# Kernel optimization log

Measured on AMD Instinct MI355X. Metric: run time of the kernel, lower is better.

Reference implementation:

```python
import jax, jax.numpy as jnp
import numpy as np

EPS = 1e-5

def _layernorm(x, gamma, beta):
    mu = jnp.mean(x, axis=-1, keepdims=True)
    var = jnp.var(x, axis=-1, keepdims=True)
    return (x - mu) * jax.lax.rsqrt(var + EPS) * gamma + beta

def setup_inputs() -> dict:
    key = jax.random.key(0)
    ks = jax.random.split(key, 8)
    B, I, H = 8192, 1024, 1024
    s_w = 1.0 / np.sqrt(I)
    s_u = 1.0 / np.sqrt(H)
    return {
        "x": jax.random.normal(ks[0], (B, I), jnp.float32),
        "h": jax.random.normal(ks[1], (B, H), jnp.float32),
        "c": jax.random.normal(ks[2], (B, H), jnp.float32),
        "W_w": jax.random.uniform(ks[3], (I, 4 * H), jnp.float32, -s_w, s_w),
        "W_b": jax.random.uniform(ks[4], (4 * H,), jnp.float32, -s_w, s_w),
        "U_w": jax.random.uniform(ks[5], (H, 4 * H), jnp.float32, -s_u, s_u),
        "ln_g_gamma": jnp.ones((4 * H,), jnp.float32),
        "ln_g_beta": jnp.zeros((4 * H,), jnp.float32),
        "ln_c_gamma": jnp.ones((H,), jnp.float32),
        "ln_c_beta": jnp.zeros((H,), jnp.float32),
    }

def reference(x, h, c, W_w, W_b, U_w, ln_g_gamma, ln_g_beta, ln_c_gamma, ln_c_beta):
    gates_x = x @ W_w + W_b            # [B, 4H]
    gates_h = h @ U_w                  # [B, 4H]
    gates = gates_x + gates_h + gates_x * gates_h  # multiplicative integration
    gates = _layernorm(gates, ln_g_gamma, ln_g_beta)
    i, f, g, o = jnp.split(gates, 4, axis=-1)
    i = jax.nn.sigmoid(i)
    f = jax.nn.sigmoid(f)
    o = jax.nn.sigmoid(o)
    g = jnp.tanh(g)
    c_new = f * c + i * g
    c_new = _layernorm(c_new, ln_c_gamma, ln_c_beta)
    h_new = o * jnp.tanh(c_new)
    return (h_new, h_new, c_new)
```

## Files before the change

### kernel.cpp

```cpp
#include <hip/hip_runtime.h>
#include <hip/hip_fp16.h>
#include <cstdint>


#define MB (1024ull * 1024ull)

typedef short bf16x8 __attribute__((ext_vector_type(8)));
typedef float f32x4  __attribute__((ext_vector_type(4)));

__device__ __forceinline__ bool bf16_mode(const void* g1) {
    return ((const unsigned short*)g1)[0] == 0x3F80u;
}
__device__ __forceinline__ float b2f(unsigned short u) {
    union { unsigned int i; float f; } v; v.i = ((unsigned int)u) << 16; return v.f;
}
__device__ __forceinline__ unsigned short f2b(float f) {
    unsigned int i = __float_as_uint(f);
    unsigned int r = (i + 0x7FFFu + ((i >> 16) & 1u)) >> 16;
    return (unsigned short)r;
}
__device__ __forceinline__ unsigned short f2h(float f) {
    __half h = __float2half_rn(f);
    return *(unsigned short*)&h;
}
__device__ __forceinline__ void uph8(uint4 v, float* o) {
    unsigned int w[4] = { v.x, v.y, v.z, v.w };
#pragma unroll
    for (int q = 0; q < 4; ++q) {
        __half2 h = *(__half2*)&w[q];
        float2 f = __half22float2(h);
        o[2 * q] = f.x; o[2 * q + 1] = f.y;
    }
}
__device__ __forceinline__ void up4(uint2 v, float* o) {
    o[0] = __uint_as_float(v.x << 16);
    o[1] = __uint_as_float(v.x & 0xFFFF0000u);
    o[2] = __uint_as_float(v.y << 16);
    o[3] = __uint_as_float(v.y & 0xFFFF0000u);
}
__device__ __forceinline__ unsigned int pack2(unsigned short a, unsigned short b) {
    return (unsigned int)a | ((unsigned int)b << 16);
}
__device__ __forceinline__ void ld4(const void* p, size_t idx, bool isbf, float* o) {
    if (isbf) up4(*(const uint2*)((const unsigned short*)p + idx), o);
    else { float4 v = *(const float4*)((const float*)p + idx); o[0]=v.x; o[1]=v.y; o[2]=v.z; o[3]=v.w; }
}
__device__ __forceinline__ float fast_sigmoid(float z) { return 1.f / (1.f + __expf(-z)); }
__device__ __forceinline__ float fast_tanh(float z)    { return 1.f - 2.f / (__expf(2.f * z) + 1.f); }

__device__ __forceinline__ void load_lds16(const unsigned short* g, unsigned short* l) {
    __builtin_amdgcn_global_load_lds(
        (const __attribute__((address_space(1))) unsigned int*)g,
        (__attribute__((address_space(3))) unsigned int*)l,
        16, 0, 0);
}

__global__ __launch_bounds__(256)
void prep_weights(const void* __restrict__ Ww, const void* __restrict__ Uw,
                  const void* __restrict__ g1,
                  unsigned short* __restrict__ Wt, unsigned short* __restrict__ Ut)
{
    const bool isbf = bf16_mode(g1);
    const void* src = blockIdx.z ? Uw : Ww;
    unsigned short* dst = blockIdx.z ? Ut : Wt;
    __shared__ unsigned short tile[64][68];
    const int t  = threadIdx.x;
    const int tx = t & 15;
    const int ty = t >> 4;
    const int bx = blockIdx.x * 64;
    const int by = blockIdx.y * 64;
    if (isbf) {
        const unsigned short* s = (const unsigned short*)src;
#pragma unroll
        for (int it = 0; it < 4; ++it) {
            const int r = ty + it * 16;
            uint2 v = *(const uint2*)(s + (size_t)(by + r) * 4096 + bx + tx * 4);
            tile[r][tx * 4 + 0] = (unsigned short)(v.x & 0xFFFFu);
            tile[r][tx * 4 + 1] = (unsigned short)(v.x >> 16);
            tile[r][tx * 4 + 2] = (unsigned short)(v.y & 0xFFFFu);
            tile[r][tx * 4 + 3] = (unsigned short)(v.y >> 16);
        }
    } else {
        const float* s = (const float*)src;
#pragma unroll
        for (int it = 0; it < 4; ++it) {
            const int r = ty + it * 16;
            float4 v = *(const float4*)(s + (size_t)(by + r) * 4096 + bx + tx * 4);
            tile[r][tx * 4 + 0] = f2b(v.x);
            tile[r][tx * 4 + 1] = f2b(v.y);
            tile[r][tx * 4 + 2] = f2b(v.z);
            tile[r][tx * 4 + 3] = f2b(v.w);
        }
    }
    __syncthreads();
#pragma unroll
    for (int it = 0; it < 4; ++it) {
        const int rn = ty + it * 16;
        const int ck = tx * 4;
        uint2 w;
        w.x = pack2(tile[ck + 0][rn], tile[ck + 1][rn]);
        w.y = pack2(tile[ck + 2][rn], tile[ck + 3][rn]);
        *(uint2*)(dst + (size_t)(bx + rn) * 1024 + by + ck) = w;
    }
}

__global__ __launch_bounds__(256)
void prep_xh(const void* __restrict__ X, const void* __restrict__ Hs,
             const void* __restrict__ g1, void* __restrict__ outb)
{
    if (bf16_mode(g1)) return;
    const float* src = (blockIdx.y == 0) ? (const float*)X : (const float*)Hs;
    unsigned short* dst = (unsigned short*)((char*)outb + (blockIdx.y == 0 ? 48 * MB : 80 * MB));
    const size_t i0 = ((size_t)blockIdx.x * 256 + threadIdx.x) * 8;
    float4 a = *(const float4*)(src + i0);
    float4 b = *(const float4*)(src + i0 + 4);
    uint4 o;
    o.x = pack2(f2b(a.x), f2b(a.y));
    o.y = pack2(f2b(a.z), f2b(a.w));
    o.z = pack2(f2b(b.x), f2b(b.y));
    o.w = pack2(f2b(b.z), f2b(b.w));
    *(uint4*)(dst + i0) = o;
}

__global__ __launch_bounds__(512, 2)
void milstm_gemm(const void* __restrict__ Xraw, const void* __restrict__ Hraw,
                 const void* __restrict__ g1, const void* __restrict__ outb,
                 const unsigned short* __restrict__ Wt,
                 const unsigned short* __restrict__ Ut,
                 unsigned short* __restrict__ Gx, unsigned short* __restrict__ Gh,
                 int m0)
{
    const bool isbf = bf16_mode(g1);
    const int  z    = blockIdx.z;
    const unsigned short* A = z
        ? (isbf ? (const unsigned short*)Hraw : (const unsigned short*)((const char*)outb + 80 * MB))
        : (isbf ? (const unsigned short*)Xraw : (const unsigned short*)((const char*)outb + 48 * MB));
    const unsigned short* Bm = z ? Ut : Wt;
    unsigned short* Gout = z ? Gh : Gx;

    __shared__ __align__(16) unsigned short lds[4][2][8192];

    const int t    = threadIdx.x;
    const int wave = t >> 6;
    const int lane = t & 63;
    const int quad = lane >> 4;
    const int l16  = lane & 15;
    const int wm2  = wave >> 2;
    const int wn4  = wave & 3;

    const int nwg  = gridDim.x * gridDim.y;
    const int wgid = blockIdx.y * gridDim.x + blockIdx.x;
    const int swz  = (wgid & 7) * (nwg >> 3) + (wgid >> 3);
    const int bm   = (swz >> 4) * 256;
    const int bn   = (swz & 15) * 256;

    const int kbsw = (((t & 3) ^ ((t >> 3) & 3)) * 8);
    const unsigned short* sa0 = A  + (size_t)(m0 + bm + (t >> 2)) * 1024 + kbsw;
    const unsigned short* sb0 = Bm + (size_t)(bn + (t >> 2)) * 1024 + kbsw;

#define STAGE(tile, buf) do {                                        \
        const int ko_ = (tile) * 32;                                 \
        load_lds16(sa0 + ko_,          &lds[buf][0][t * 8]);         \
        load_lds16(sa0 + 131072 + ko_, &lds[buf][0][4096 + t * 8]);  \
        load_lds16(sb0 + ko_,          &lds[buf][1][t * 8]);         \
        load_lds16(sb0 + 131072 + ko_, &lds[buf][1][4096 + t * 8]);  \
    } while (0)

    const int kread = (quad ^ ((l16 >> 1) & 3)) * 8;
    const int raoff = (wm2 * 128 + l16) * 32 + kread;
    const int rboff = (wn4 * 64 + l16) * 32 + kread;

    f32x4 acc[8][4] = {};

    STAGE(0, 0);
    STAGE(1, 1);
    STAGE(2, 2);

    for (int q = 0; q < 32; ++q) {
        const int buf = q & 3;
        asm volatile("s_waitcnt vmcnt(8)" ::: "memory");
        __builtin_amdgcn_s_barrier();
        __builtin_amdgcn_sched_barrier(0);
        STAGE((q + 3) & 31, (q + 3) & 3);

        const unsigned short* pA = &lds[buf][0][0];
        const unsigned short* pB = &lds[buf][1][0];
        bf16x8 b[4], a[8];
#pragma unroll
        for (int ni = 0; ni < 4; ++ni) b[ni] = *(const bf16x8*)(pB + rboff + ni * 512);
#pragma unroll
        for (int mi = 0; mi < 8; ++mi) a[mi] = *(const bf16x8*)(pA + raoff + mi * 512);

        __builtin_amdgcn_s_setprio(1);
#pragma unroll
        for (int mi = 0; mi < 8; ++mi)
#pragma unroll
            for (int ni = 0; ni < 4; ++ni)
                acc[mi][ni] = __builtin_amdgcn_mfma_f32_16x16x32_bf16(a[mi], b[ni], acc[mi][ni], 0, 0, 0);
        __builtin_amdgcn_s_setprio(0);
    }
#undef STAGE

    const int col0 = bn + wn4 * 64 + l16;
#pragma unroll
    for (int mi = 0; mi < 8; ++mi) {
        const int row0 = bm + wm2 * 128 + mi * 16 + quad * 4;
#pragma unroll
        for (int ni = 0; ni < 4; ++ni) {
            const int col = col0 + ni * 16;
#pragma unroll
            for (int r = 0; r < 4; ++r)
                Gout[(size_t)(row0 + r) * 4096 + col] = f2h(acc[mi][ni][r]);
        }
    }
}

__global__ __launch_bounds__(256)
void milstm_cell(const unsigned short* __restrict__ Gx,
                 const unsigned short* __restrict__ Gh,
                 const void* __restrict__ Wbr,
                 const void* __restrict__ C,
                 const void* __restrict__ g1, const void* __restrict__ b1,
                 const void* __restrict__ g2, const void* __restrict__ b2,
                 void* __restrict__ outb, int m0)
{
    const bool isbf = bf16_mode(g1);
    const int lrow = blockIdx.x;
    const int row  = m0 + lrow;
    const int tid  = threadIdx.x;
    const int lane = tid & 63;
    const int wave = tid >> 6;
    const uint4* gx4 = (const uint4*)(Gx + (size_t)lrow * 4096);
    const uint4* gh4 = (const uint4*)(Gh + (size_t)lrow * 4096);

    __shared__ __align__(16) float srow[4096];
    __shared__ float red[16];

    float s = 0.f, ss = 0.f;
#pragma unroll
    for (int u = 0; u < 2; ++u) {
        const int gbase = (tid * 2 + u) * 8;
        float fx[8], fh[8], bb[8];
        uph8(gx4[tid * 2 + u], fx);
        uph8(gh4[tid * 2 + u], fh);
        ld4(Wbr, gbase, isbf, bb);
        ld4(Wbr, gbase + 4, isbf, bb + 4);
        float g[8];
#pragma unroll
        for (int k = 0; k < 8; ++k) {
            const float ax = fx[k] + bb[k];
            const float v  = ax + fh[k] + ax * fh[k];
            g[k] = v;
            s  += v;
            ss += v * v;
        }
        *(float4*)&srow[gbase]     = make_float4(g[0], g[1], g[2], g[3]);
        *(float4*)&srow[gbase + 4] = make_float4(g[4], g[5], g[6], g[7]);
    }
#pragma unroll
    for (int off = 32; off > 0; off >>= 1) {
        s  += __shfl_xor(s, off, 64);
        ss += __shfl_xor(ss, off, 64);
    }
    if (lane == 0) { red[wave] = s; red[8 + wave] = ss; }
    __syncthreads();
    s  = red[0] + red[1] + red[2] + red[3];
    ss = red[8] + red[9] + red[10] + red[11];
    const float mu   = s * (1.f / 4096.f);
    const float rstd = rsqrtf(fmaxf(ss * (1.f / 4096.f) - mu * mu, 0.f) + 1e-5f);

    const int j0 = tid * 4;
    float xi[4], xf[4], xg[4], cc[4];
    float G1[4], B1[4], ii[4], cn[4], ov[4];

    { float4 v = *(const float4*)&srow[j0];        xi[0]=v.x; xi[1]=v.y; xi[2]=v.z; xi[3]=v.w; }
    { float4 v = *(const float4*)&srow[1024 + j0]; xf[0]=v.x; xf[1]=v.y; xf[2]=v.z; xf[3]=v.w; }
    { float4 v = *(const float4*)&srow[2048 + j0]; xg[0]=v.x; xg[1]=v.y; xg[2]=v.z; xg[3]=v.w; }
    { float4 v = *(const float4*)&srow[3072 + j0]; ov[0]=v.x; ov[1]=v.y; ov[2]=v.z; ov[3]=v.w; }
    ld4(C, (size_t)row * 1024 + j0, isbf, cc);

    ld4(g1, j0, isbf, G1); ld4(b1, j0, isbf, B1);
#pragma unroll
    for (int q = 0; q < 4; ++q) ii[q] = fast_sigmoid((xi[q] - mu) * rstd * G1[q] + B1[q]);
    ld4(g1, 1024 + j0, isbf, G1); ld4(b1, 1024 + j0, isbf, B1);
#pragma unroll
    for (int q = 0; q < 4; ++q) xf[q] = fast_sigmoid((xf[q] - mu) * rstd * G1[q] + B1[q]);
    ld4(g1, 2048 + j0, isbf, G1); ld4(b1, 2048 + j0, isbf, B1);
#pragma unroll
    for (int q = 0; q < 4; ++q) xg[q] = fast_tanh((xg[q] - mu) * rstd * G1[q] + B1[q]);
    ld4(g1, 3072 + j0, isbf, G1); ld4(b1, 3072 + j0, isbf, B1);
#pragma unroll
    for (int q = 0; q < 4; ++q) ov[q] = fast_sigmoid((ov[q] - mu) * rstd * G1[q] + B1[q]);
#pragma unroll
    for (int q = 0; q < 4; ++q) cn[q] = xf[q] * cc[q] + ii[q] * xg[q];

    float s2  = cn[0] + cn[1] + cn[2] + cn[3];
    float ss2 = cn[0]*cn[0] + cn[1]*cn[1] + cn[2]*cn[2] + cn[3]*cn[3];
#pragma unroll
    for (int off = 32; off > 0; off >>= 1) {
        s2  += __shfl_xor(s2, off, 64);
        ss2 += __shfl_xor(ss2, off, 64);
    }
    if (lane == 0) { red[4 + wave] = s2; red[12 + wave] = ss2; }
    __syncthreads();
    s2  = red[4]  + red[5]  + red[6]  + red[7];
    ss2 = red[12] + red[13] + red[14] + red[15];
    const float mu2   = s2 * (1.f / 1024.f);
    const float rstd2 = rsqrtf(fmaxf(ss2 * (1.f / 1024.f) - mu2 * mu2, 0.f) + 1e-5f);

    ld4(g2, j0, isbf, G1);
    ld4(b2, j0, isbf, B1);

    float hv[4], cv[4];
#pragma unroll
    for (int q = 0; q < 4; ++q) {
        cv[q] = (cn[q] - mu2) * rstd2 * G1[q] + B1[q];
        hv[q] = ov[q] * fast_tanh(cv[q]);
    }

    const size_t BH = (size_t)8192 * 1024;
    if (isbf) {
        unsigned short* out = (unsigned short*)outb;
        uint2 hb, cb;
        hb.x = pack2(f2b(hv[0]), f2b(hv[1])); hb.y = pack2(f2b(hv[2]), f2b(hv[3]));
        cb.x = pack2(f2b(cv[0]), f2b(cv[1])); cb.y = pack2(f2b(cv[2]), f2b(cv[3]));
        *(uint2*)(out + (size_t)row * 1024 + j0)          = hb;
        *(uint2*)(out + BH + (size_t)row * 1024 + j0)     = hb;
        *(uint2*)(out + 2 * BH + (size_t)row * 1024 + j0) = cb;
    } else {
        float* out = (float*)outb;
        float4 hf = { hv[0], hv[1], hv[2], hv[3] };
        float4 cf = { cv[0], cv[1], cv[2], cv[3] };
        *(float4*)(out + (size_t)row * 1024 + j0)          = hf;
        *(float4*)(out + BH + (size_t)row * 1024 + j0)     = hf;
        *(float4*)(out + 2 * BH + (size_t)row * 1024 + j0) = cf;
    }
}

extern "C" void kernel_launch(void* const* d_in, const int* in_sizes, int n_in,
                              void* d_out, int out_size, void* d_ws, size_t ws_size,
                              hipStream_t stream)
{
    const void* X  = d_in[0];
    const void* Hh = d_in[1];
    const void* C  = d_in[2];
    const void* Ww = d_in[3];
    const void* Wb = d_in[4];
    const void* Uw = d_in[5];
    const void* g1 = d_in[6];
    const void* b1 = d_in[7];
    const void* g2 = d_in[8];
    const void* b2 = d_in[9];

    const int P  = (ws_size >= 144 * MB) ? 1 : ((ws_size >= 80 * MB) ? 2 : 4);
    const int MR = 8192 / P;
    const size_t gsz = (size_t)MR * 4096;
    unsigned short* Gx = (unsigned short*)d_ws;
    unsigned short* Gh = Gx + gsz;
    unsigned short* Wt = Gh + gsz;
    unsigned short* Ut = Wt + (size_t)4096 * 1024;

    prep_weights<<<dim3(64, 16, 2), 256, 0, stream>>>(Ww, Uw, g1, Wt, Ut);
    prep_xh<<<dim3(4096, 2), 256, 0, stream>>>(X, Hh, g1, d_out);

    for (int ph = 0; ph < P; ++ph) {
        const int m0 = ph * MR;
        milstm_gemm<<<dim3(16, MR / 256, 2), 512, 0, stream>>>(
            X, Hh, g1, d_out, Wt, Ut, Gx, Gh, m0);
        milstm_cell<<<dim3(MR), 256, 0, stream>>>(
            Gx, Gh, Wb, C, g1, b1, g2, b2, d_out, m0);
    }
}
```

Measured before the change: 408.6 us.

## Restructure GEMM main loop into 8-phase ping-pong schedule with 64-wide K tiles

```diff
diff --git a/kernel.cpp b/kernel.cpp
--- a/kernel.cpp
+++ b/kernel.cpp
@@ -138,15 +138,16 @@
     const unsigned short* Bm = z ? Ut : Wt;
     unsigned short* Gout = z ? Gh : Gx;
 
-    __shared__ __align__(16) unsigned short lds[4][2][8192];
+    __shared__ __align__(16) unsigned short ldsA[2][2][8192];
+    __shared__ __align__(16) unsigned short ldsB[2][2][8192];
 
     const int t    = threadIdx.x;
     const int wave = t >> 6;
     const int lane = t & 63;
     const int quad = lane >> 4;
     const int l16  = lane & 15;
-    const int wm2  = wave >> 2;
-    const int wn4  = wave & 3;
+    const int wm   = wave >> 2;
+    const int wn   = wave & 3;
 
     const int nwg  = gridDim.x * gridDim.y;
     const int wgid = blockIdx.y * gridDim.x + blockIdx.x;
@@ -154,57 +155,119 @@
     const int bm   = (swz >> 4) * 256;
     const int bn   = (swz & 15) * 256;
 
-    const int kbsw = (((t & 3) ^ ((t >> 3) & 3)) * 8);
-    const unsigned short* sa0 = A  + (size_t)(m0 + bm + (t >> 2)) * 1024 + kbsw;
-    const unsigned short* sb0 = Bm + (size_t)(bn + (t >> 2)) * 1024 + kbsw;
-
-#define STAGE(tile, buf) do {                                        \
-        const int ko_ = (tile) * 32;                                 \
-        load_lds16(sa0 + ko_,          &lds[buf][0][t * 8]);         \
-        load_lds16(sa0 + 131072 + ko_, &lds[buf][0][4096 + t * 8]);  \
-        load_lds16(sb0 + ko_,          &lds[buf][1][t * 8]);         \
-        load_lds16(sb0 + 131072 + ko_, &lds[buf][1][4096 + t * 8]);  \
+    const int gls = (((t & 7) ^ ((t >> 3) & 7)) * 8);
+    const unsigned short* pA = A  + (size_t)(m0 + bm + (t >> 3)) * 1024 + gls;
+    const unsigned short* pB = Bm + (size_t)(bn + (t >> 3)) * 1024 + gls;
+
+#define ST_A(DB, H, KO) do {                                                  \
+        load_lds16(pA + (H) * 131072 + (KO),         &ldsA[DB][H][t * 8]);    \
+        load_lds16(pA + (H) * 131072 + 65536 + (KO), &ldsA[DB][H][4096 + t * 8]); \
     } while (0)
-
-    const int kread = (quad ^ ((l16 >> 1) & 3)) * 8;
-    const int raoff = (wm2 * 128 + l16) * 32 + kread;
-    const int rboff = (wn4 * 64 + l16) * 32 + kread;
+#define ST_B(DB, H, KO) do {                                                  \
+        load_lds16(pB + (H) * 131072 + (KO),         &ldsB[DB][H][t * 8]);    \
+        load_lds16(pB + (H) * 131072 + 65536 + (KO), &ldsB[DB][H][4096 + t * 8]); \
+    } while (0)
+
+    const int gp0 = ((quad)     ^ (l16 & 7)) * 8;
+    const int gp1 = ((4 + quad) ^ (l16 & 7)) * 8;
+    const unsigned short* bA0 = &ldsA[0][wm][0] + l16 * 64;
+    const unsigned short* bA1 = &ldsA[1][wm][0] + l16 * 64;
+    const unsigned short* bB0 = &ldsB[0][wn >> 1][0] + (wn & 1) * 4096 + l16 * 64;
+    const unsigned short* bB1 = &ldsB[1][wn >> 1][0] + (wn & 1) * 4096 + l16 * 64;
+
+#define LD_AF(BASE) do { _Pragma("unroll")                                    \
+        for (int j = 0; j < 4; ++j) {                                         \
+            aF[j * 2 + 0] = *(const bf16x8*)((BASE) + j * 1024 + gp0);        \
+            aF[j * 2 + 1] = *(const bf16x8*)((BASE) + j * 1024 + gp1);        \
+        } } while (0)
+#define LD_BF(BASE, DST) do { _Pragma("unroll")                               \
+        for (int n = 0; n < 2; ++n) {                                         \
+            DST[n * 2 + 0] = *(const bf16x8*)((BASE) + n * 1024 + gp0);       \
+            DST[n * 2 + 1] = *(const bf16x8*)((BASE) + n * 1024 + gp1);       \
+        } } while (0)
+
+#define BAR()   __builtin_amdgcn_s_barrier()
+#define LGKM0() do { asm volatile("s_waitcnt lgkmcnt(0)" ::: "memory");       \
+                     __builtin_amdgcn_sched_barrier(0); } while (0)
+#define MFMA16(MBASE, NBASE, BV) do {                                         \
+        __builtin_amdgcn_s_setprio(1);                                        \
+        _Pragma("unroll")                                                     \
+        for (int j = 0; j < 4; ++j)                                           \
+            _Pragma("unroll")                                                 \
+            for (int n = 0; n < 2; ++n)                                       \
+                _Pragma("unroll")                                             \
+                for (int ks = 0; ks < 2; ++ks)                                \
+                    acc[(MBASE) + j][(NBASE) + n] =                           \
+                        __builtin_amdgcn_mfma_f32_16x16x32_bf16(              \
+                            aF[j * 2 + ks], BV[n * 2 + ks],                   \
+                            acc[(MBASE) + j][(NBASE) + n], 0, 0, 0);          \
+        __builtin_amdgcn_s_setprio(0);                                        \
+    } while (0)
 
     f32x4 acc[8][4] = {};
-
-    STAGE(0, 0);
-    STAGE(1, 1);
-    STAGE(2, 2);
-
-    for (int q = 0; q < 32; ++q) {
-        const int buf = q & 3;
-        asm volatile("s_waitcnt vmcnt(8)" ::: "memory");
-        __builtin_amdgcn_s_barrier();
-        __builtin_amdgcn_sched_barrier(0);
-        STAGE((q + 3) & 31, (q + 3) & 3);
-
-        const unsigned short* pA = &lds[buf][0][0];
-        const unsigned short* pB = &lds[buf][1][0];
-        bf16x8 b[4], a[8];
-#pragma unroll
-        for (int ni = 0; ni < 4; ++ni) b[ni] = *(const bf16x8*)(pB + rboff + ni * 512);
-#pragma unroll
-        for (int mi = 0; mi < 8; ++mi) a[mi] = *(const bf16x8*)(pA + raoff + mi * 512);
-
-        __builtin_amdgcn_s_setprio(1);
-#pragma unroll
-        for (int mi = 0; mi < 8; ++mi)
-#pragma unroll
-            for (int ni = 0; ni < 4; ++ni)
-                acc[mi][ni] = __builtin_amdgcn_mfma_f32_16x16x32_bf16(a[mi], b[ni], acc[mi][ni], 0, 0, 0);
-        __builtin_amdgcn_s_setprio(0);
-    }
-#undef STAGE
-
-    const int col0 = bn + wn4 * 64 + l16;
+    bf16x8 aF[8], bL[4], bH[4];
+
+    ST_A(0, 0, 0);  ST_B(0, 0, 0);  ST_B(0, 1, 0);  ST_A(0, 1, 0);
+    ST_A(1, 0, 64); ST_B(1, 0, 64); ST_B(1, 1, 64);
+    asm volatile("s_waitcnt vmcnt(6)" ::: "memory");
+    BAR();
+
+    for (int i = 0; i < 8; ++i) {
+        const int kt1 = (128 * i + 64)  & 1023;
+        const int kt2 = (128 * i + 128) & 1023;
+        const int kt3 = (128 * i + 192) & 1023;
+
+        LD_AF(bA0); LD_BF(bB0, bL);
+        ST_A(1, 1, kt1);
+        BAR(); LGKM0();
+        MFMA16(0, 0, bL);
+        BAR();
+        LD_BF(bB0 + 2048, bH);
+        BAR(); LGKM0();
+        MFMA16(0, 2, bH);
+        BAR();
+        LD_AF(bA0 + 4096);
+        ST_B(0, 0, kt2);
+        BAR(); LGKM0();
+        MFMA16(4, 2, bH);
+        BAR();
+        ST_B(0, 1, kt2); ST_A(0, 0, kt2);
+        BAR(); LGKM0();
+        MFMA16(4, 0, bL);
+        asm volatile("s_waitcnt vmcnt(6)" ::: "memory");
+        BAR();
+        LD_AF(bA1); LD_BF(bB1, bL);
+        ST_A(0, 1, kt2);
+        BAR(); LGKM0();
+        MFMA16(0, 0, bL);
+        BAR();
+        LD_BF(bB1 + 2048, bH);
+        BAR(); LGKM0();
+        MFMA16(0, 2, bH);
+        BAR();
+        LD_AF(bA1 + 4096);
+        ST_B(1, 0, kt3);
+        BAR(); LGKM0();
+        MFMA16(4, 2, bH);
+        BAR();
+        ST_B(1, 1, kt3); ST_A(1, 0, kt3);
+        BAR(); LGKM0();
+        MFMA16(4, 0, bL);
+        asm volatile("s_waitcnt vmcnt(6)" ::: "memory");
+        BAR();
+    }
+#undef ST_A
+#undef ST_B
+#undef LD_AF
+#undef LD_BF
+#undef BAR
+#undef LGKM0
+#undef MFMA16
+
+    const int col0 = bn + wn * 64 + l16;
 #pragma unroll
     for (int mi = 0; mi < 8; ++mi) {
-        const int row0 = bm + wm2 * 128 + mi * 16 + quad * 4;
+        const int row0 = bm + wm * 128 + mi * 16 + quad * 4;
 #pragma unroll
         for (int ni = 0; ni < 4; ++ni) {
             const int col = col0 + ni * 16;
```

After: 418.5 us. +2.4%, slower.

## Double-buffer LDS fragments in registers to overlap LDS reads with MFMA

Applied to the files above, without the earlier changes.

```diff
diff --git a/kernel.cpp b/kernel.cpp
--- a/kernel.cpp
+++ b/kernel.cpp
@@ -170,36 +170,63 @@
     const int raoff = (wm2 * 128 + l16) * 32 + kread;
     const int rboff = (wn4 * 64 + l16) * 32 + kread;
 
+#define LDA(DST, BUF) do { _Pragma("unroll")                                  \
+        for (int mi = 0; mi < 8; ++mi)                                        \
+            DST[mi] = *(const bf16x8*)(&lds[BUF][0][0] + raoff + mi * 512);   \
+    } while (0)
+#define LDB(DST, BUF) do { _Pragma("unroll")                                  \
+        for (int ni = 0; ni < 4; ++ni)                                        \
+            DST[ni] = *(const bf16x8*)(&lds[BUF][1][0] + rboff + ni * 512);   \
+    } while (0)
+
+#define BAR()  __builtin_amdgcn_s_barrier()
+#define VM4()  asm volatile("s_waitcnt vmcnt(4)" ::: "memory")
+#define MFMA32(AV, BV) do {                                                   \
+        __builtin_amdgcn_s_setprio(1);                                        \
+        _Pragma("unroll")                                                     \
+        for (int mi = 0; mi < 8; ++mi)                                        \
+            _Pragma("unroll")                                                 \
+            for (int ni = 0; ni < 4; ++ni)                                    \
+                acc[mi][ni] = __builtin_amdgcn_mfma_f32_16x16x32_bf16(        \
+                    AV[mi], BV[ni], acc[mi][ni], 0, 0, 0);                    \
+        __builtin_amdgcn_s_setprio(0);                                        \
+    } while (0)
+
     f32x4 acc[8][4] = {};
+    bf16x8 aP[8], bP[4], aQ[8], bQ[4];
 
     STAGE(0, 0);
     STAGE(1, 1);
     STAGE(2, 2);
-
-    for (int q = 0; q < 32; ++q) {
-        const int buf = q & 3;
-        asm volatile("s_waitcnt vmcnt(8)" ::: "memory");
-        __builtin_amdgcn_s_barrier();
-        __builtin_amdgcn_sched_barrier(0);
-        STAGE((q + 3) & 31, (q + 3) & 3);
-
-        const unsigned short* pA = &lds[buf][0][0];
-        const unsigned short* pB = &lds[buf][1][0];
-        bf16x8 b[4], a[8];
-#pragma unroll
-        for (int ni = 0; ni < 4; ++ni) b[ni] = *(const bf16x8*)(pB + rboff + ni * 512);
-#pragma unroll
-        for (int mi = 0; mi < 8; ++mi) a[mi] = *(const bf16x8*)(pA + raoff + mi * 512);
-
-        __builtin_amdgcn_s_setprio(1);
-#pragma unroll
-        for (int mi = 0; mi < 8; ++mi)
-#pragma unroll
-            for (int ni = 0; ni < 4; ++ni)
-                acc[mi][ni] = __builtin_amdgcn_mfma_f32_16x16x32_bf16(a[mi], b[ni], acc[mi][ni], 0, 0, 0);
-        __builtin_amdgcn_s_setprio(0);
+    asm volatile("s_waitcnt vmcnt(8)" ::: "memory");
+    BAR();
+    LDA(aP, 0); LDB(bP, 0);
+
+    for (int ii = 0; ii < 8; ++ii) {
+        const int q = 4 * ii;
+        VM4(); BAR();
+        STAGE((q + 3) & 31, 3);
+        LDA(aQ, 1); LDB(bQ, 1);
+        MFMA32(aP, bP);
+        VM4(); BAR();
+        STAGE((q + 4) & 31, 0);
+        LDA(aP, 2); LDB(bP, 2);
+        MFMA32(aQ, bQ);
+        VM4(); BAR();
+        STAGE((q + 5) & 31, 1);
+        LDA(aQ, 3); LDB(bQ, 3);
+        MFMA32(aP, bP);
+        VM4(); BAR();
+        STAGE((q + 6) & 31, 2);
+        LDA(aP, 0); LDB(bP, 0);
+        MFMA32(aQ, bQ);
     }
 #undef STAGE
+#undef LDA
+#undef LDB
+#undef BAR
+#undef VM4
+#undef MFMA32
 
     const int col0 = bn + wn4 * 64 + l16;
 #pragma unroll
```

New measurement: 417.7 us. 2.2% more time.
